# Optimization experiments

Measured on AMD Instinct MI355X. Metric: run time of the kernel, lower is better.

Reference implementation:

```python
import jax, jax.numpy as jnp
import numpy as np

D, M, B, K = 512, 128, 16, 4
COHERENCE_COEFF = 0.01
LAMBDA_COEFF = 1.0


def setup_inputs() -> dict:
    key = jax.random.key(0)
    k1, k2, k3, k4 = jax.random.split(key, 4)
    x = jax.random.normal(k1, (2, 2048, D), dtype=jnp.float32)
    V = jax.random.normal(k2, (D, M, B), dtype=jnp.float32)
    U = jax.random.normal(k3, (M, D, B), dtype=jnp.float32)
    u_scales = jax.random.normal(k4, (M, B), dtype=jnp.float32)
    return {"x": x, "V": V, "U": U, "u_scales": u_scales}


def _forward(x, V, U, u_scales):
    # UnitColNorm parametrizations: normalize over the D axis
    Vn = V / jnp.linalg.norm(V, axis=0, keepdims=True)          # (D, m, b)
    Un = U / jnp.linalg.norm(U, axis=1, keepdims=True)          # (m, D, b)
    s = jnp.tanh(u_scales) * LAMBDA_COEFF                        # (m, b)
    U_eff = Un * s[:, None, :]                                   # (m, D, b)

    expert_reprs = jnp.einsum('...d,dmb->...mb', x, Vn)          # (..., m, b)
    repr_l2_sq = jnp.sum(expert_reprs * expert_reprs, axis=-1)   # (..., m)
    topk_vals, topk_idxs = jax.lax.top_k(repr_l2_sq, K)          # (..., k)

    reprs_topk = jnp.take_along_axis(expert_reprs, topk_idxs[..., None], axis=-2)  # (..., k, b)
    U_active = U_eff[topk_idxs]                                  # (..., k, D, b)
    writes = jnp.einsum('...kdb,...kb->...d', U_active, reprs_topk)

    # aux terms
    N = topk_vals.size // K
    idxs_flat = topk_idxs.reshape(-1)
    vals_flat = topk_vals.reshape(-1)
    energy_per_expert = jnp.zeros((M,), dtype=vals_flat.dtype).at[idxs_flat].add(vals_flat) / N
    select_rate = jnp.zeros((M,), dtype=vals_flat.dtype).at[idxs_flat].add(1.0) / N
    total_energy = jnp.maximum(energy_per_expert.sum(), 1e-12)
    relative_energy = energy_per_expert / total_energy

    eye = jnp.eye(M * B, dtype=Vn.dtype)
    sqrtD = jnp.sqrt(jnp.asarray(D, dtype=Vn.dtype))

    def coherence_penalty(Mtx):
        G = Mtx.T @ Mtx  # (m*b, m*b)
        return jnp.abs(G - eye).mean() * sqrtD

    v_pen = coherence_penalty(Vn.reshape(D, M * B))
    u_pen = coherence_penalty(U_eff.transpose(1, 0, 2).reshape(D, M * B))
    aux_loss = COHERENCE_COEFF * v_pen - total_energy

    out = x + writes
    return (out, total_energy, energy_per_expert, relative_energy,
            select_rate, v_pen, u_pen, aux_loss)


def reference(x, V, U, u_scales):
    return _forward(x, V, U, u_scales)
```

## Files before the change

kernel.cpp:

```cpp
#include <hip/hip_runtime.h>
#include <math.h>

#define D 512
#define M 128
#define B 16
#define KSEL 4
#define NC 2048
#define NTOK 4096

typedef unsigned short ushort;
typedef unsigned int uint;
typedef unsigned long long u64;
typedef __attribute__((ext_vector_type(8))) short short8;
typedef __attribute__((ext_vector_type(4))) float floatx4;

#define WS_EACC   0
#define WS_CACC   128
#define WS_VSUM   256
#define WS_USUM   257
#define WS_CNT_I  258
#define WS_VSCALE 512
#define WS_USCALE 2560
#define WS_E_F    4608
#define WS_RBF_F  528896
#define WS_XH_F   2626048
#define WS_XL_F   3674624
#define WS_VHT_F  4723200
#define WS_VLT_F  5247488
#define WS_UHT_F  5771776
#define WS_ULT_F  6296064
#define WS_LIST_F 6820352

#define OUT_TE   2097152
#define OUT_EPE  2097153
#define OUT_RE   2097281
#define OUT_SR   2097409
#define OUT_VPEN 2097537
#define OUT_UPEN 2097538
#define OUT_AUX  2097539

#define GLDS16(g, l) __builtin_amdgcn_global_load_lds(                        \
    (const __attribute__((address_space(1))) unsigned int*)(g),               \
    (__attribute__((address_space(3))) unsigned int*)(l), 16, 0, 0)

__device__ __forceinline__ ushort f2bf(float f) {
    union { float f; uint u; } a; a.f = f;
    uint u = a.u;
    u += 0x7fffu + ((u >> 16) & 1u);
    return (ushort)(u >> 16);
}
__device__ __forceinline__ float bf2f(ushort h) {
    union { uint u; float f; } a; a.u = ((uint)h) << 16;
    return a.f;
}

__launch_bounds__(256)
__global__ void prep_kernel(const float* __restrict__ x, const float* __restrict__ V,
                            const float* __restrict__ U, const float* __restrict__ us_in,
                            ushort* __restrict__ xh, ushort* __restrict__ xl,
                            ushort* __restrict__ vht, ushort* __restrict__ vlt,
                            ushort* __restrict__ uht, ushort* __restrict__ ult,
                            float* __restrict__ ws) {
    __shared__ float ts[64][65];
    const int bid = blockIdx.x;
    const int tid = threadIdx.x;

    if (bid < 1024) {
        const int idx = (bid * 256 + tid) * 8;
        float4 v0 = *(const float4*)(x + idx);
        float4 v1 = *(const float4*)(x + idx + 4);
        float vv[8] = {v0.x, v0.y, v0.z, v0.w, v1.x, v1.y, v1.z, v1.w};
        union { ushort u[8]; uint4 q; } H, L;
#pragma unroll
        for (int j = 0; j < 8; ++j) {
            ushort h = f2bf(vv[j]);
            H.u[j] = h;
            L.u[j] = f2bf(vv[j] - bf2f(h));
        }
        *(uint4*)(xh + idx) = H.q;
        *(uint4*)(xl + idx) = L.q;
    } else if (bid < 1280) {
        const int vb = bid - 1024;
        const int col0 = (vb & 31) * 64;
        const int d0 = (vb >> 5) * 64;
#pragma unroll
        for (int i = 0; i < 16; ++i) {
            int idx = i * 256 + tid;
            int r = idx >> 6, c = idx & 63;
            ts[r][c] = V[(size_t)(d0 + r) * NC + col0 + c];
        }
        __syncthreads();
#pragma unroll
        for (int i = 0; i < 16; ++i) {
            int idx = i * 256 + tid;
            int c2 = idx >> 6, d2 = idx & 63;
            float v = ts[d2][c2];
            ushort h = f2bf(v);
            vht[(size_t)(col0 + c2) * D + d0 + d2] = h;
            vlt[(size_t)(col0 + c2) * D + d0 + d2] = f2bf(v - bf2f(h));
        }
    } else if (bid < 1408) {
        const int m = bid - 1280;
        float (*t2)[129] = (float (*)[129])ts;
        for (int d0 = 0; d0 < D; d0 += 128) {
            __syncthreads();
#pragma unroll
            for (int i = 0; i < 8; ++i) {
                int idx = i * 256 + tid;
                int d2 = idx >> 4, b2 = idx & 15;
                t2[b2][d2] = U[(size_t)m * (D * B) + (size_t)(d0 + d2) * B + b2];
            }
            __syncthreads();
#pragma unroll
            for (int i = 0; i < 8; ++i) {
                int idx = i * 256 + tid;
                int b3 = idx >> 7, d3 = idx & 127;
                float v = t2[b3][d3];
                ushort h = f2bf(v);
                uht[(size_t)((m << 4) + b3) * D + d0 + d3] = h;
                ult[(size_t)((m << 4) + b3) * D + d0 + d3] = f2bf(v - bf2f(h));
            }
        }
    } else {
        const int bx = bid - 1408;
        if (bx >= 160) {
            ws[(bx - 160) * 256 + tid] = 0.0f;
            return;
        }
        if (bx < 32) {
            const int c = bx * 64 + (tid & 63);
            const int dg = tid >> 6;
            float s = 0.0f;
            for (int d = dg; d < D; d += 4) {
                float v = V[(size_t)d * NC + c];
                s = fmaf(v, v, s);
            }
            float (*sh)[64] = (float (*)[64])ts;
            sh[dg][tid & 63] = s;
            __syncthreads();
            if (tid < 64) {
                float t = (sh[0][tid] + sh[1][tid]) + (sh[2][tid] + sh[3][tid]);
                ws[WS_VSCALE + bx * 64 + tid] = 1.0f / sqrtf(t);
            }
        } else {
            const int m = bx - 32;
            const float* p = U + (size_t)m * (D * B);
            float s = 0.0f;
            for (int i = tid; i < D * B; i += 256) {
                float v = p[i];
                s = fmaf(v, v, s);
            }
            float* sh2 = &ts[0][0];
            sh2[tid] = s;
            __syncthreads();
            if (tid < 16) {
                float t = 0.0f;
#pragma unroll
                for (int j = 0; j < 16; ++j) t += sh2[tid + (j << 4)];
                ws[WS_USCALE + (m << 4) + tid] = tanhf(us_in[(m << 4) + tid]) / sqrtf(t);
            }
        }
    }
}

__launch_bounds__(256)
__global__ void mfma_fused(const ushort* __restrict__ xh, const ushort* __restrict__ xl,
                           const ushort* __restrict__ vht, const ushort* __restrict__ vlt,
                           const ushort* __restrict__ uht, const ushort* __restrict__ ult,
                           float* __restrict__ ws, ushort* __restrict__ rbf) {
    __shared__ ushort smem[16384];
    const int bid = blockIdx.x;
    const int tid = threadIdx.x, lane = tid & 63, w = tid >> 6;
    const int wr = w >> 1, wc = w & 1;
    const int r15 = lane & 15, q = lane >> 4;
    const int srl = lane >> 2;
    const int skq = (lane & 3) ^ ((lane >> 3) & 3);
    const int perm8 = (q ^ ((r15 >> 1) & 3)) * 8;

    const int is_gemm = bid < 512;
    const ushort* srcs[4];
    int rbase[4];
    int gi = 0, gj = 0, which = 0;
    if (is_gemm) {
        const int tokB = (bid & 31) * 128, colB = (bid >> 5) * 128;
        srcs[0] = xh; srcs[1] = xl; srcs[2] = vht; srcs[3] = vlt;
        rbase[0] = tokB; rbase[1] = tokB; rbase[2] = colB; rbase[3] = colB;
    } else {
        int t = bid - 512;
        which = t >= 136;
        if (which) t -= 136;
        int bi = 0, rem = 16;
        while (t >= rem) { t -= rem; --rem; ++bi; }
        gi = bi; gj = bi + t;
        const ushort* ht = which ? uht : vht;
        srcs[0] = ht; srcs[1] = ht; srcs[2] = ht; srcs[3] = ht;
        rbase[0] = gi * 128; rbase[1] = gi * 128; rbase[2] = gj * 128; rbase[3] = gj * 128;
    }

    floatx4 acc[4][4];
#pragma unroll
    for (int i = 0; i < 4; ++i)
#pragma unroll
        for (int j = 0; j < 4; ++j) acc[i][j] = (floatx4){0.f, 0.f, 0.f, 0.f};

    auto stage = [&](int c) {
        const int kb = c * 32 + skq * 8;
#pragma unroll
        for (int tI = 0; tI < 4; ++tI) {
            if (!is_gemm && (tI & 1)) continue;
            const ushort* s = srcs[tI] + (size_t)rbase[tI] * D + kb;
#pragma unroll
            for (int sub = 0; sub < 2; ++sub) {
                const int row16 = w * 32 + sub * 16;
                GLDS16(s + (size_t)(row16 + srl) * D,
                       &smem[tI * 4096 + row16 * 32]);
            }
        }
    };

    stage(0);
    for (int c = 0; c < 16; ++c) {
        __syncthreads();
        short8 ah[4], al[4], bh[4], bl[4];
#pragma unroll
        for (int s = 0; s < 4; ++s) {
            const int ra = (wr * 64 + s * 16 + r15) * 32 + perm8;
            ah[s] = *(const short8*)&smem[ra];
            const int rb = (wc * 64 + s * 16 + r15) * 32 + perm8;
            bh[s] = *(const short8*)&smem[8192 + rb];
            if (is_gemm) {
                al[s] = *(const short8*)&smem[4096 + ra];
                bl[s] = *(const short8*)&smem[12288 + rb];
            }
        }
        __syncthreads();
        if (c < 15) stage(c + 1);
#pragma unroll
        for (int st = 0; st < 4; ++st)
#pragma unroll
            for (int sc = 0; sc < 4; ++sc) {
                acc[st][sc] = __builtin_amdgcn_mfma_f32_16x16x32_bf16(ah[st], bh[sc], acc[st][sc], 0, 0, 0);
                if (is_gemm) {
                    acc[st][sc] = __builtin_amdgcn_mfma_f32_16x16x32_bf16(ah[st], bl[sc], acc[st][sc], 0, 0, 0);
                    acc[st][sc] = __builtin_amdgcn_mfma_f32_16x16x32_bf16(al[st], bh[sc], acc[st][sc], 0, 0, 0);
                }
            }
    }

    if (is_gemm) {
        const int tok0 = (bid & 31) * 128 + wr * 64, col0 = (bid >> 5) * 128 + wc * 64;
#pragma unroll
        for (int sc = 0; sc < 4; ++sc) {
            const int colg = col0 + sc * 16 + r15;
            const float vs = ws[WS_VSCALE + colg];
            const int ex = colg >> 4;
#pragma unroll
            for (int st = 0; st < 4; ++st) {
                const int rowb = tok0 + st * 16 + q * 4;
                float r0 = acc[st][sc][0] * vs;
                float r1 = acc[st][sc][1] * vs;
                float r2 = acc[st][sc][2] * vs;
                float r3 = acc[st][sc][3] * vs;
                rbf[(size_t)(rowb + 0) * NC + colg] = f2bf(r0);
                rbf[(size_t)(rowb + 1) * NC + colg] = f2bf(r1);
                rbf[(size_t)(rowb + 2) * NC + colg] = f2bf(r2);
                rbf[(size_t)(rowb + 3) * NC + colg] = f2bf(r3);
                float e0 = r0 * r0, e1 = r1 * r1, e2 = r2 * r2, e3 = r3 * r3;
#pragma unroll
                for (int mk = 1; mk < 16; mk <<= 1) {
                    e0 += __shfl_xor(e0, mk);
                    e1 += __shfl_xor(e1, mk);
                    e2 += __shfl_xor(e2, mk);
                    e3 += __shfl_xor(e3, mk);
                }
                if (r15 == 0) {
                    float* ep = ws + WS_E_F + (size_t)rowb * M + ex;
                    ep[0] = e0; ep[M] = e1; ep[2 * M] = e2; ep[3 * M] = e3;
                }
            }
        }
    } else {
        const float* scl = ws + (which ? WS_USCALE : WS_VSCALE);
        float* sum_out = ws + (which ? WS_USUM : WS_VSUM);
        float local = 0.0f;
#pragma unroll
        for (int sc = 0; sc < 4; ++sc) {
            const int colg = gj * 128 + wc * 64 + sc * 16 + r15;
            const float scj = scl[colg];
#pragma unroll
            for (int st = 0; st < 4; ++st) {
#pragma unroll
                for (int reg = 0; reg < 4; ++reg) {
                    const int rowg = gi * 128 + wr * 64 + st * 16 + q * 4 + reg;
                    float g = acc[st][sc][reg] * scl[rowg] * scj;
                    if (rowg == colg) g -= 1.0f;
                    local += fabsf(g);
                }
            }
        }
        if (gi < gj) local *= 2.0f;
#pragma unroll
        for (int mk = 1; mk < 64; mk <<= 1) local += __shfl_xor(local, mk);
        __shared__ float red[4];
        if (lane == 0) red[w] = local;
        __syncthreads();
        if (tid == 0) atomicAdd(sum_out, (red[0] + red[1]) + (red[2] + red[3]));
    }
}

__launch_bounds__(256)
__global__ void topk_kernel(float* __restrict__ ws) {
    const int tid = threadIdx.x, lane = tid & 63, w = tid >> 6;
    const int t = blockIdx.x * 4 + w;
    int* icnt = (int*)ws + WS_CNT_I;
    int* ilist = (int*)(ws + WS_LIST_F);

    const float2 ev = *(const float2*)(ws + WS_E_F + (size_t)t * M + lane * 2);
    const uint i0 = (uint)(lane * 2), i1 = i0 + 1;
    u64 k0 = ((u64)__float_as_uint(ev.x) << 32) | (uint)(~i0);
    u64 k1 = ((u64)__float_as_uint(ev.y) << 32) | (uint)(~i1);
    u64 s0 = k0 > k1 ? k0 : k1;
    u64 s1 = k0 > k1 ? k1 : k0;
    u64 s2 = 0, s3 = 0;

#pragma unroll
    for (int mk = 1; mk < 64; mk <<= 1) {
        u64 o0 = __shfl_xor(s0, mk);
        u64 o1 = __shfl_xor(s1, mk);
        u64 o2 = __shfl_xor(s2, mk);
        u64 o3 = __shfl_xor(s3, mk);
        u64 c0 = s0 > o3 ? s0 : o3;
        u64 c1 = s1 > o2 ? s1 : o2;
        u64 c2 = s2 > o1 ? s2 : o1;
        u64 c3 = s3 > o0 ? s3 : o0;
        u64 d0 = c0 > c2 ? c0 : c2, d2 = c0 > c2 ? c2 : c0;
        u64 d1 = c1 > c3 ? c1 : c3, d3 = c1 > c3 ? c3 : c1;
        s0 = d0 > d1 ? d0 : d1; s1 = d0 > d1 ? d1 : d0;
        s2 = d2 > d3 ? d2 : d3; s3 = d2 > d3 ? d3 : d2;
    }

    if (lane < 4) {
        u64 key = (lane == 0) ? s0 : (lane == 1) ? s1 : (lane == 2) ? s2 : s3;
        const int e = (int)(~(uint)key);
        const float val = __uint_as_float((uint)(key >> 32));
        atomicAdd(&ws[WS_EACC + e], val);
        atomicAdd(&ws[WS_CACC + e], 1.0f);
        int pos = atomicAdd(&icnt[e], 1);
        ilist[(e << 12) + pos] = (t << 2) | lane;
    }
}

__launch_bounds__(256)
__global__ void expert_contrib_kernel(const float* __restrict__ U,
                                      const ushort* __restrict__ rbf,
                                      const float* __restrict__ ws,
                                      uint* __restrict__ contrib) {
    const int e = blockIdx.x;
    const int tid = threadIdx.x;
    const int cnt = ((const int*)ws)[WS_CNT_I + e];
    if ((int)blockIdx.y >= cnt) return;

    float usc[16];
#pragma unroll
    for (int b = 0; b < 16; ++b) usc[b] = ws[WS_USCALE + (e << 4) + b];

    const float* Up = U + (size_t)e * (D * B);
    float u0[16], u1[16];
#pragma unroll
    for (int qd = 0; qd < 4; ++qd) {
        float4 a = *(const float4*)(Up + (size_t)(2 * tid) * B + qd * 4);
        float4 b4 = *(const float4*)(Up + (size_t)(2 * tid + 1) * B + qd * 4);
        u0[qd * 4 + 0] = a.x * usc[qd * 4 + 0];
        u0[qd * 4 + 1] = a.y * usc[qd * 4 + 1];
        u0[qd * 4 + 2] = a.z * usc[qd * 4 + 2];
        u0[qd * 4 + 3] = a.w * usc[qd * 4 + 3];
        u1[qd * 4 + 0] = b4.x * usc[qd * 4 + 0];
        u1[qd * 4 + 1] = b4.y * usc[qd * 4 + 1];
        u1[qd * 4 + 2] = b4.z * usc[qd * 4 + 2];
        u1[qd * 4 + 3] = b4.w * usc[qd * 4 + 3];
    }

    const int* ilist = (const int*)(ws + WS_LIST_F) + (e << 12);
    int i = blockIdx.y;
    int pk = (i < cnt) ? ilist[i] : 0;
    while (i < cnt) {
        const int t = pk >> 2, k = pk & 3;
        const ushort* rp = rbf + (size_t)t * NC + (e << 4);
        union { ushort u[16]; uint4 q[2]; } R;
        R.q[0] = *(const uint4*)(rp);
        R.q[1] = *(const uint4*)(rp + 8);
        const int inext = i + 4;
        if (inext < cnt) pk = ilist[inext];
        float acc0 = 0.0f, acc1 = 0.0f;
#pragma unroll
        for (int b = 0; b < 16; ++b) {
            const float wv = bf2f(R.u[b]);
            acc0 = fmaf(u0[b], wv, acc0);
            acc1 = fmaf(u1[b], wv, acc1);
        }
        contrib[(size_t)((t << 2) + k) * 256 + tid] =
            (uint)f2bf(acc0) | ((uint)f2bf(acc1) << 16);
        i = inext;
    }
}

__launch_bounds__(256)
__global__ void combine_kernel(const float* __restrict__ x,
                               const uint* __restrict__ contrib,
                               const float* __restrict__ ws,
                               float* __restrict__ out) {
    if (blockIdx.x == 1024) {
        const int m = threadIdx.x;
        if (m >= 128) return;
        float e = ws[WS_EACC + m] * (1.0f / (float)NTOK);
        float c = ws[WS_CACC + m] * (1.0f / (float)NTOK);
        float s = e;
#pragma unroll
        for (int off = 32; off > 0; off >>= 1) s += __shfl_down(s, off);
        __shared__ float sh[2];
        if ((m & 63) == 0) sh[m >> 6] = s;
        __syncthreads();
        float total = sh[0] + sh[1];
        float total_energy = fmaxf(total, 1e-12f);
        out[OUT_EPE + m] = e;
        out[OUT_RE + m] = e / total_energy;
        out[OUT_SR + m] = c;
        if (m == 0) {
            out[OUT_TE] = total_energy;
            float inv_n2 = 1.0f / ((float)NC * (float)NC);
            float sqrtD = sqrtf((float)D);
            float vpen = ws[WS_VSUM] * inv_n2 * sqrtD;
            float upen = ws[WS_USUM] * inv_n2 * sqrtD;
            out[OUT_VPEN] = vpen;
            out[OUT_UPEN] = upen;
            out[OUT_AUX] = 0.01f * vpen - total_energy;
        }
        return;
    }

    const int gid = blockIdx.x * 256 + threadIdx.x;
    const int t = gid >> 6;
    const int dq = (gid & 63) << 3;
    const uint4* cp = (const uint4*)contrib;

    float s[8];
    float4 x0 = *(const float4*)(x + (size_t)t * D + dq);
    float4 x1 = *(const float4*)(x + (size_t)t * D + dq + 4);
    s[0] = x0.x; s[1] = x0.y; s[2] = x0.z; s[3] = x0.w;
    s[4] = x1.x; s[5] = x1.y; s[6] = x1.z; s[7] = x1.w;
#pragma unroll
    for (int k = 0; k < KSEL; ++k) {
        uint4 cvec = cp[(size_t)((t << 2) + k) * 64 + (dq >> 3)];
        uint cc[4] = {cvec.x, cvec.y, cvec.z, cvec.w};
#pragma unroll
        for (int j = 0; j < 4; ++j) {
            s[2 * j]     += bf2f((ushort)(cc[j] & 0xffffu));
            s[2 * j + 1] += bf2f((ushort)(cc[j] >> 16));
        }
    }
    float* op = out + (size_t)t * D + dq;
    *(float4*)(op)     = make_float4(s[0], s[1], s[2], s[3]);
    *(float4*)(op + 4) = make_float4(s[4], s[5], s[6], s[7]);
}

extern "C" void kernel_launch(void* const* d_in, const int* in_sizes, int n_in,
                              void* d_out, int out_size, void* d_ws, size_t ws_size,
                              hipStream_t stream) {
    const float* x  = (const float*)d_in[0];
    const float* V  = (const float*)d_in[1];
    const float* U  = (const float*)d_in[2];
    const float* us = (const float*)d_in[3];
    float* out = (float*)d_out;
    float* ws  = (float*)d_ws;

    ushort* xh  = (ushort*)(ws + WS_XH_F);
    ushort* xl  = (ushort*)(ws + WS_XL_F);
    ushort* vht = (ushort*)(ws + WS_VHT_F);
    ushort* vlt = (ushort*)(ws + WS_VLT_F);
    ushort* uht = (ushort*)(ws + WS_UHT_F);
    ushort* ult = (ushort*)(ws + WS_ULT_F);
    ushort* rbf = (ushort*)(ws + WS_RBF_F);
    uint* contrib = (uint*)(ws + WS_XH_F);

    prep_kernel<<<1570, 256, 0, stream>>>(x, V, U, us, xh, xl, vht, vlt, uht, ult, ws);
    mfma_fused<<<784, 256, 0, stream>>>(xh, xl, vht, vlt, uht, ult, ws, rbf);
    topk_kernel<<<NTOK / 4, 256, 0, stream>>>(ws);
    expert_contrib_kernel<<<dim3(128, 4), 256, 0, stream>>>(U, rbf, ws, contrib);
    combine_kernel<<<1025, 256, 0, stream>>>(x, contrib, ws, out);
}
```

Baseline: 195.3 us.

## Double-buffer A tile in LDS and load B fragments directly from global

After: 217.4 us. 11.3% more time.

```diff
diff --git a/kernel.cpp b/kernel.cpp
--- a/kernel.cpp
+++ b/kernel.cpp
@@ -178,13 +178,12 @@
     const int perm8 = (q ^ ((r15 >> 1) & 3)) * 8;
 
     const int is_gemm = bid < 512;
-    const ushort* srcs[4];
-    int rbase[4];
+    const ushort *aH, *aL, *bH, *bL;
+    int arow, brow;
     int gi = 0, gj = 0, which = 0;
     if (is_gemm) {
-        const int tokB = (bid & 31) * 128, colB = (bid >> 5) * 128;
-        srcs[0] = xh; srcs[1] = xl; srcs[2] = vht; srcs[3] = vlt;
-        rbase[0] = tokB; rbase[1] = tokB; rbase[2] = colB; rbase[3] = colB;
+        arow = (bid & 31) * 128; brow = (bid >> 5) * 128;
+        aH = xh; aL = xl; bH = vht; bL = vlt;
     } else {
         int t = bid - 512;
         which = t >= 136;
@@ -193,8 +192,8 @@
         while (t >= rem) { t -= rem; --rem; ++bi; }
         gi = bi; gj = bi + t;
         const ushort* ht = which ? uht : vht;
-        srcs[0] = ht; srcs[1] = ht; srcs[2] = ht; srcs[3] = ht;
-        rbase[0] = gi * 128; rbase[1] = gi * 128; rbase[2] = gj * 128; rbase[3] = gj * 128;
+        aH = ht; aL = ht; bH = ht; bL = ht;
+        arow = gi * 128; brow = gj * 128;
     }
 
     floatx4 acc[4][4];
@@ -203,38 +202,42 @@
 #pragma unroll
         for (int j = 0; j < 4; ++j) acc[i][j] = (floatx4){0.f, 0.f, 0.f, 0.f};
 
-    auto stage = [&](int c) {
+    auto stageA = [&](int buf, int c) {
         const int kb = c * 32 + skq * 8;
 #pragma unroll
-        for (int tI = 0; tI < 4; ++tI) {
-            if (!is_gemm && (tI & 1)) continue;
-            const ushort* s = srcs[tI] + (size_t)rbase[tI] * D + kb;
-#pragma unroll
-            for (int sub = 0; sub < 2; ++sub) {
-                const int row16 = w * 32 + sub * 16;
-                GLDS16(s + (size_t)(row16 + srl) * D,
-                       &smem[tI * 4096 + row16 * 32]);
-            }
+        for (int sub = 0; sub < 2; ++sub) {
+            const int row16 = w * 32 + sub * 16;
+            GLDS16(aH + (size_t)(arow + row16 + srl) * D + kb,
+                   &smem[buf * 8192 + row16 * 32]);
+            if (is_gemm)
+                GLDS16(aL + (size_t)(arow + row16 + srl) * D + kb,
+                       &smem[buf * 8192 + 4096 + row16 * 32]);
         }
     };
 
-    stage(0);
+    const ushort* bHp = bH + (size_t)(brow + wc * 64 + r15) * D + q * 8;
+    const ushort* bLp = bL + (size_t)(brow + wc * 64 + r15) * D + q * 8;
+
+    stageA(0, 0);
     for (int c = 0; c < 16; ++c) {
         __syncthreads();
-        short8 ah[4], al[4], bh[4], bl[4];
+        short8 bh[4], bl[4];
+#pragma unroll
+        for (int s = 0; s < 4; ++s) {
+            bh[s] = *(const short8*)(bHp + (size_t)(s * 16) * D + c * 32);
+            if (is_gemm) bl[s] = *(const short8*)(bLp + (size_t)(s * 16) * D + c * 32);
+        }
+        __builtin_amdgcn_sched_barrier(0);
+        if (c < 15) stageA((c + 1) & 1, c + 1);
+        __builtin_amdgcn_sched_barrier(0);
+        const ushort* bp = &smem[(c & 1) * 8192];
+        short8 ah[4], al[4];
 #pragma unroll
         for (int s = 0; s < 4; ++s) {
             const int ra = (wr * 64 + s * 16 + r15) * 32 + perm8;
-            ah[s] = *(const short8*)&smem[ra];
-            const int rb = (wc * 64 + s * 16 + r15) * 32 + perm8;
-            bh[s] = *(const short8*)&smem[8192 + rb];
-            if (is_gemm) {
-                al[s] = *(const short8*)&smem[4096 + ra];
-                bl[s] = *(const short8*)&smem[12288 + rb];
-            }
-        }
-        __syncthreads();
-        if (c < 15) stage(c + 1);
+            ah[s] = *(const short8*)&bp[ra];
+            if (is_gemm) al[s] = *(const short8*)&bp[4096 + ra];
+        }
 #pragma unroll
         for (int st = 0; st < 4; ++st)
 #pragma unroll
@@ -248,7 +251,7 @@
     }
 
     if (is_gemm) {
-        const int tok0 = (bid & 31) * 128 + wr * 64, col0 = (bid >> 5) * 128 + wc * 64;
+        const int tok0 = arow + wr * 64, col0 = brow + wc * 64;
 #pragma unroll
         for (int sc = 0; sc < 4; ++sc) {
             const int colg = col0 + sc * 16 + r15;
```
